# Kernel optimization log

Hardware: AMD Instinct MI355X
Metric: run time of the kernel (lower is better)

## Reference

```python
import jax, jax.numpy as jnp
import numpy as np

N_NODES = 100000
N_HYPEREDGES = 10000
NNZ = 1600000

def setup_inputs() -> dict:
    key = jax.random.key(0)
    k = jax.random.split(key, 7)
    return {
        "x": jax.random.normal(k[0], (N_NODES, 1), dtype=jnp.float32),
        "W1": jax.random.normal(k[1], (1, 128), dtype=jnp.float32) * 0.5,
        "b1": jax.random.normal(k[2], (128,), dtype=jnp.float32) * 0.1,
        "W2": jax.random.normal(k[3], (128, 1), dtype=jnp.float32) * 0.1,
        "b2": jax.random.normal(k[4], (1,), dtype=jnp.float32) * 0.1,
        "node_idx": jax.random.randint(k[5], (NNZ,), 0, N_NODES, dtype=jnp.int64),
        "edge_idx": jax.random.randint(k[6], (NNZ,), 0, N_HYPEREDGES, dtype=jnp.int64),
    }

def _hypergraph_conv(x, W, b, node_idx, edge_idx, n_nodes, n_edges):
    # PyG HypergraphConv (use_attention=False, hyperedge_weight=1):
    # out = D^-1 H B^-1 H^T (X W) + b
    x = x @ W  # [N, F_out]
    ones = jnp.ones(node_idx.shape[0], dtype=x.dtype)
    D = jax.ops.segment_sum(ones, node_idx, num_segments=n_nodes)   # node degree
    B = jax.ops.segment_sum(ones, edge_idx, num_segments=n_edges)   # hyperedge degree
    D_inv = jnp.where(D > 0, 1.0 / D, 0.0)
    B_inv = jnp.where(B > 0, 1.0 / B, 0.0)
    # node -> hyperedge: e = B^-1 H^T x
    e = B_inv[:, None] * jax.ops.segment_sum(x[node_idx], edge_idx, num_segments=n_edges)
    # hyperedge -> node: out = D^-1 H e
    out = D_inv[:, None] * jax.ops.segment_sum(e[edge_idx], node_idx, num_segments=n_nodes)
    return out + b

def reference(x, W1, b1, W2, b2, node_idx, edge_idx):
    n_nodes = x.shape[0]
    h = _hypergraph_conv(x, W1, b1, node_idx, edge_idx, n_nodes, N_HYPEREDGES)
    h = jax.nn.relu(h)
    out = _hypergraph_conv(h, W2, b2, node_idx, edge_idx, n_nodes, N_HYPEREDGES)
    return out
```

## Files before the change

### kernel.cpp

```cpp
#include <hip/hip_runtime.h>

static constexpr int N_NODES = 100000;
static constexpr int N_EDGES = 10000;
static constexpr int NNZ     = 1600000;

static constexpr int G1    = 256;
static constexpr int CHUNK = NNZ / G1;
static constexpr int NRN   = 250;
static constexpr int RN    = 400;
static constexpr int NRE   = 250;
static constexpr int RE    = 40;
static constexpr int SLOT  = 64;
static constexpr int BLK   = 1024;
static constexpr int NW    = BLK / 64;


__global__ __launch_bounds__(BLK) void k_bin(
        const int* __restrict__ nidx, const int* __restrict__ eidx,
        unsigned* __restrict__ binN, unsigned* __restrict__ binE,
        unsigned* __restrict__ cntN, unsigned* __restrict__ cntE) {
    __shared__ unsigned cN[NRN], cE[NRE];
    for (int j = threadIdx.x; j < NRN; j += BLK) cN[j] = 0u;
    for (int j = threadIdx.x; j < NRE; j += BLK) cE[j] = 0u;
    __syncthreads();
    const int b = blockIdx.x;
    const int i0 = b * CHUNK, i1 = i0 + CHUNK;
    for (int i = i0 + threadIdx.x; i < i1; i += BLK) {
        int n = nidx[i], e = eidx[i];
        int rn = n / RN;
        int re = e / RE;
        unsigned pn = atomicAdd(&cN[rn], 1u);
        unsigned pe = atomicAdd(&cE[re], 1u);
        binN[((size_t)rn * G1 + b) * SLOT + pn] = ((unsigned)(n - rn * RN) << 14) | (unsigned)e;
        binE[((size_t)re * G1 + b) * SLOT + pe] = ((unsigned)(e - re * RE) << 17) | (unsigned)n;
    }
    __syncthreads();
    for (int j = threadIdx.x; j < NRN; j += BLK) cntN[(size_t)j * G1 + b] = cN[j];
    for (int j = threadIdx.x; j < NRE; j += BLK) cntE[(size_t)j * G1 + b] = cE[j];
}

__global__ __launch_bounds__(BLK) void k_edge1(
        const unsigned* __restrict__ binE, const unsigned* __restrict__ cntE,
        const float* __restrict__ x,
        float* __restrict__ Binv, float* __restrict__ v1) {
    __shared__ float    sS[NW][RE];
    __shared__ unsigned sC[NW][RE];
    __shared__ unsigned scnt[G1];
    const int t = threadIdx.x;
    for (int j = t; j < NW * RE; j += BLK) { ((float*)sS)[j] = 0.0f; ((unsigned*)sC)[j] = 0u; }
    if (t < G1) scnt[t] = cntE[(size_t)blockIdx.x * G1 + t];
    __syncthreads();
    const int wv = t >> 6;
    const unsigned* base = binE + (size_t)blockIdx.x * G1 * SLOT;
    for (int j = t; j < G1 * SLOT; j += BLK) {
        int s = j & (SLOT - 1), bb = j >> 6;
        if ((unsigned)s < scnt[bb]) {
            unsigned w = base[j];
            unsigned el = w >> 17;
            unsigned n  = w & 0x1FFFFu;
            atomicAdd(&sS[wv][el], x[n]);
            atomicAdd(&sC[wv][el], 1u);
        }
    }
    __syncthreads();
    if (t < RE) {
        float s = 0.0f; unsigned c = 0u;
        #pragma unroll
        for (int k = 0; k < NW; ++k) { s += sS[k][t]; c += sC[k][t]; }
        float binv = (c > 0u) ? (1.0f / (float)c) : 0.0f;
        int e = blockIdx.x * RE + t;
        Binv[e] = binv;
        v1[e]   = s * binv;
    }
}

__global__ __launch_bounds__(BLK) void k_node1_mlp(
        const unsigned* __restrict__ binN, const unsigned* __restrict__ cntN,
        const float* __restrict__ v1,
        const float* __restrict__ W1, const float* __restrict__ b1,
        const float* __restrict__ W2,
        float* __restrict__ Dinv, float* __restrict__ y) {
    __shared__ float    sV[N_EDGES];
    __shared__ float    sS[RN];
    __shared__ unsigned sC[RN];
    __shared__ unsigned scnt[G1];
    __shared__ float    wgt[384];
    for (int j = threadIdx.x; j < N_EDGES; j += BLK) sV[j] = v1[j];
    if (threadIdx.x < RN) { sS[threadIdx.x] = 0.0f; sC[threadIdx.x] = 0u; }
    if (threadIdx.x < G1) scnt[threadIdx.x] = cntN[(size_t)blockIdx.x * G1 + threadIdx.x];
    if (threadIdx.x < 128) {
        wgt[threadIdx.x]       = W1[threadIdx.x];
        wgt[128 + threadIdx.x] = b1[threadIdx.x];
        wgt[256 + threadIdx.x] = W2[threadIdx.x];
    }
    __syncthreads();
    const unsigned* base = binN + (size_t)blockIdx.x * G1 * SLOT;
    for (int j = threadIdx.x; j < G1 * SLOT; j += BLK) {
        int s = j & (SLOT - 1), bb = j >> 6;
        if ((unsigned)s < scnt[bb]) {
            unsigned w = base[j];
            unsigned nl = w >> 14;
            atomicAdd(&sS[nl], sV[w & 0x3FFFu]);
            atomicAdd(&sC[nl], 1u);
        }
    }
    __syncthreads();
    if (threadIdx.x < RN) {
        unsigned c = sC[threadIdx.x];
        float dinv = (c > 0u) ? (1.0f / (float)c) : 0.0f;
        int n = blockIdx.x * RN + threadIdx.x;
        Dinv[n] = dinv;
        float tt = sS[threadIdx.x] * dinv;
        float acc = 0.0f;
        #pragma unroll
        for (int f = 0; f < 128; ++f) {
            float h = fmaf(tt, wgt[f], wgt[128 + f]);
            h = fmaxf(h, 0.0f);
            acc = fmaf(h, wgt[256 + f], acc);
        }
        y[n] = acc;
    }
}

__global__ __launch_bounds__(BLK) void k_edge2(
        const unsigned* __restrict__ binE, const unsigned* __restrict__ cntE,
        const float* __restrict__ y, const float* __restrict__ Binv,
        float* __restrict__ v2) {
    __shared__ float    sS[NW][RE];
    __shared__ unsigned scnt[G1];
    const int t = threadIdx.x;
    for (int j = t; j < NW * RE; j += BLK) ((float*)sS)[j] = 0.0f;
    if (t < G1) scnt[t] = cntE[(size_t)blockIdx.x * G1 + t];
    __syncthreads();
    const int wv = t >> 6;
    const unsigned* base = binE + (size_t)blockIdx.x * G1 * SLOT;
    for (int j = t; j < G1 * SLOT; j += BLK) {
        int s = j & (SLOT - 1), bb = j >> 6;
        if ((unsigned)s < scnt[bb]) {
            unsigned w = base[j];
            atomicAdd(&sS[wv][w >> 17], y[w & 0x1FFFFu]);
        }
    }
    __syncthreads();
    if (t < RE) {
        float s = 0.0f;
        #pragma unroll
        for (int k = 0; k < NW; ++k) s += sS[k][t];
        int e = blockIdx.x * RE + t;
        v2[e] = s * Binv[e];
    }
}

__global__ __launch_bounds__(BLK) void k_node2_final(
        const unsigned* __restrict__ binN, const unsigned* __restrict__ cntN,
        const float* __restrict__ v2, const float* __restrict__ Dinv,
        const float* __restrict__ b2, float* __restrict__ out) {
    __shared__ float    sV[N_EDGES];
    __shared__ float    sS[RN];
    __shared__ unsigned scnt[G1];
    for (int j = threadIdx.x; j < N_EDGES; j += BLK) sV[j] = v2[j];
    if (threadIdx.x < RN) sS[threadIdx.x] = 0.0f;
    if (threadIdx.x < G1) scnt[threadIdx.x] = cntN[(size_t)blockIdx.x * G1 + threadIdx.x];
    __syncthreads();
    const unsigned* base = binN + (size_t)blockIdx.x * G1 * SLOT;
    for (int j = threadIdx.x; j < G1 * SLOT; j += BLK) {
        int s = j & (SLOT - 1), bb = j >> 6;
        if ((unsigned)s < scnt[bb]) {
            unsigned w = base[j];
            atomicAdd(&sS[w >> 14], sV[w & 0x3FFFu]);
        }
    }
    __syncthreads();
    if (threadIdx.x < RN) {
        int n = blockIdx.x * RN + threadIdx.x;
        out[n] = fmaf(sS[threadIdx.x], Dinv[n], b2[0]);
    }
}

extern "C" void kernel_launch(void* const* d_in, const int* in_sizes, int n_in,
                              void* d_out, int out_size, void* d_ws, size_t ws_size,
                              hipStream_t stream) {
    const float* x    = (const float*)d_in[0];
    const float* W1   = (const float*)d_in[1];
    const float* b1   = (const float*)d_in[2];
    const float* W2   = (const float*)d_in[3];
    const float* b2   = (const float*)d_in[4];
    const int*   nidx = (const int*)d_in[5];
    const int*   eidx = (const int*)d_in[6];
    float*       out  = (float*)d_out;

    char* ws = (char*)d_ws;
    unsigned* binN = (unsigned*)(ws + 0);
    unsigned* binE = (unsigned*)(ws + 16384000);
    unsigned* cntN = (unsigned*)(ws + 32768000);
    unsigned* cntE = (unsigned*)(ws + 33024000);
    float*    v1   = (float*)(ws + 33280000);
    float*    v2   = v1 + N_EDGES;
    float*    Binv = v2 + N_EDGES;
    float*    Dinv = Binv + N_EDGES;
    float*    y    = Dinv + N_NODES;

    k_bin          <<<G1,  BLK, 0, stream>>>(nidx, eidx, binN, binE, cntN, cntE);
    k_edge1        <<<NRE, BLK, 0, stream>>>(binE, cntE, x, Binv, v1);
    k_node1_mlp    <<<NRN, BLK, 0, stream>>>(binN, cntN, v1, W1, b1, W2, Dinv, y);
    k_edge2        <<<NRE, BLK, 0, stream>>>(binE, cntE, y, Binv, v2);
    k_node2_final  <<<NRN, BLK, 0, stream>>>(binN, cntN, v2, Dinv, b2, out);
}
```

Before: 83.92 us.

## Fuse four propagation kernels into one persistent kernel with grid barriers

```diff
diff --git a/kernel.cpp b/kernel.cpp
--- a/kernel.cpp
+++ b/kernel.cpp
@@ -13,13 +13,28 @@
 static constexpr int SLOT  = 64;
 static constexpr int BLK   = 1024;
 static constexpr int NW    = BLK / 64;
-
+static constexpr int GF    = 256;
+
+
+__device__ __forceinline__ void grid_barrier(unsigned* bar, unsigned target) {
+    __syncthreads();
+    if (threadIdx.x == 0) {
+        __threadfence();
+        __hip_atomic_fetch_add(bar, 1u, __ATOMIC_RELEASE, __HIP_MEMORY_SCOPE_AGENT);
+        while (__hip_atomic_load(bar, __ATOMIC_RELAXED, __HIP_MEMORY_SCOPE_AGENT) < target)
+            __builtin_amdgcn_s_sleep(16);
+        __threadfence();
+    }
+    __syncthreads();
+}
 
 __global__ __launch_bounds__(BLK) void k_bin(
         const int* __restrict__ nidx, const int* __restrict__ eidx,
         unsigned* __restrict__ binN, unsigned* __restrict__ binE,
-        unsigned* __restrict__ cntN, unsigned* __restrict__ cntE) {
+        unsigned* __restrict__ cntN, unsigned* __restrict__ cntE,
+        unsigned* __restrict__ bar) {
     __shared__ unsigned cN[NRN], cE[NRE];
+    if (blockIdx.x == 0 && threadIdx.x < 4) bar[threadIdx.x] = 0u;
     for (int j = threadIdx.x; j < NRN; j += BLK) cN[j] = 0u;
     for (int j = threadIdx.x; j < NRE; j += BLK) cE[j] = 0u;
     __syncthreads();
@@ -39,141 +54,131 @@
     for (int j = threadIdx.x; j < NRE; j += BLK) cntE[(size_t)j * G1 + b] = cE[j];
 }
 
-__global__ __launch_bounds__(BLK) void k_edge1(
-        const unsigned* __restrict__ binE, const unsigned* __restrict__ cntE,
+__global__ __launch_bounds__(BLK) void k_fused(
+        const unsigned* __restrict__ binN, const unsigned* __restrict__ binE,
+        const unsigned* __restrict__ cntN, const unsigned* __restrict__ cntE,
         const float* __restrict__ x,
-        float* __restrict__ Binv, float* __restrict__ v1) {
-    __shared__ float    sS[NW][RE];
-    __shared__ unsigned sC[NW][RE];
-    __shared__ unsigned scnt[G1];
+        const float* __restrict__ W1, const float* __restrict__ b1,
+        const float* __restrict__ W2, const float* __restrict__ b2,
+        float* __restrict__ v1, float* __restrict__ v2,
+        float* __restrict__ Binv, float* __restrict__ Dinv, float* __restrict__ y,
+        unsigned* __restrict__ bar, float* __restrict__ out) {
+    __shared__ union {
+        struct { unsigned scnt[G1]; float sS[NW][RE]; unsigned sC[NW][RE]; } e;
+        struct { float sV[N_EDGES]; float sS[RN]; unsigned sC[RN]; unsigned scnt[G1];
+                 float wgt[384]; } n;
+    } sm;
+    const int b = blockIdx.x;
     const int t = threadIdx.x;
-    for (int j = t; j < NW * RE; j += BLK) { ((float*)sS)[j] = 0.0f; ((unsigned*)sC)[j] = 0u; }
-    if (t < G1) scnt[t] = cntE[(size_t)blockIdx.x * G1 + t];
-    __syncthreads();
-    const int wv = t >> 6;
-    const unsigned* base = binE + (size_t)blockIdx.x * G1 * SLOT;
-    for (int j = t; j < G1 * SLOT; j += BLK) {
-        int s = j & (SLOT - 1), bb = j >> 6;
-        if ((unsigned)s < scnt[bb]) {
-            unsigned w = base[j];
-            unsigned el = w >> 17;
-            unsigned n  = w & 0x1FFFFu;
-            atomicAdd(&sS[wv][el], x[n]);
-            atomicAdd(&sC[wv][el], 1u);
-        }
-    }
-    __syncthreads();
-    if (t < RE) {
-        float s = 0.0f; unsigned c = 0u;
-        #pragma unroll
-        for (int k = 0; k < NW; ++k) { s += sS[k][t]; c += sC[k][t]; }
-        float binv = (c > 0u) ? (1.0f / (float)c) : 0.0f;
-        int e = blockIdx.x * RE + t;
-        Binv[e] = binv;
-        v1[e]   = s * binv;
-    }
-}
-
-__global__ __launch_bounds__(BLK) void k_node1_mlp(
-        const unsigned* __restrict__ binN, const unsigned* __restrict__ cntN,
-        const float* __restrict__ v1,
-        const float* __restrict__ W1, const float* __restrict__ b1,
-        const float* __restrict__ W2,
-        float* __restrict__ Dinv, float* __restrict__ y) {
-    __shared__ float    sV[N_EDGES];
-    __shared__ float    sS[RN];
-    __shared__ unsigned sC[RN];
-    __shared__ unsigned scnt[G1];
-    __shared__ float    wgt[384];
-    for (int j = threadIdx.x; j < N_EDGES; j += BLK) sV[j] = v1[j];
-    if (threadIdx.x < RN) { sS[threadIdx.x] = 0.0f; sC[threadIdx.x] = 0u; }
-    if (threadIdx.x < G1) scnt[threadIdx.x] = cntN[(size_t)blockIdx.x * G1 + threadIdx.x];
-    if (threadIdx.x < 128) {
-        wgt[threadIdx.x]       = W1[threadIdx.x];
-        wgt[128 + threadIdx.x] = b1[threadIdx.x];
-        wgt[256 + threadIdx.x] = W2[threadIdx.x];
-    }
-    __syncthreads();
-    const unsigned* base = binN + (size_t)blockIdx.x * G1 * SLOT;
-    for (int j = threadIdx.x; j < G1 * SLOT; j += BLK) {
-        int s = j & (SLOT - 1), bb = j >> 6;
-        if ((unsigned)s < scnt[bb]) {
-            unsigned w = base[j];
-            unsigned nl = w >> 14;
-            atomicAdd(&sS[nl], sV[w & 0x3FFFu]);
-            atomicAdd(&sC[nl], 1u);
-        }
-    }
-    __syncthreads();
-    if (threadIdx.x < RN) {
-        unsigned c = sC[threadIdx.x];
-        float dinv = (c > 0u) ? (1.0f / (float)c) : 0.0f;
-        int n = blockIdx.x * RN + threadIdx.x;
-        Dinv[n] = dinv;
-        float tt = sS[threadIdx.x] * dinv;
-        float acc = 0.0f;
-        #pragma unroll
-        for (int f = 0; f < 128; ++f) {
-            float h = fmaf(tt, wgt[f], wgt[128 + f]);
-            h = fmaxf(h, 0.0f);
-            acc = fmaf(h, wgt[256 + f], acc);
-        }
-        y[n] = acc;
-    }
-}
-
-__global__ __launch_bounds__(BLK) void k_edge2(
-        const unsigned* __restrict__ binE, const unsigned* __restrict__ cntE,
-        const float* __restrict__ y, const float* __restrict__ Binv,
-        float* __restrict__ v2) {
-    __shared__ float    sS[NW][RE];
-    __shared__ unsigned scnt[G1];
-    const int t = threadIdx.x;
-    for (int j = t; j < NW * RE; j += BLK) ((float*)sS)[j] = 0.0f;
-    if (t < G1) scnt[t] = cntE[(size_t)blockIdx.x * G1 + t];
-    __syncthreads();
-    const int wv = t >> 6;
-    const unsigned* base = binE + (size_t)blockIdx.x * G1 * SLOT;
-    for (int j = t; j < G1 * SLOT; j += BLK) {
-        int s = j & (SLOT - 1), bb = j >> 6;
-        if ((unsigned)s < scnt[bb]) {
-            unsigned w = base[j];
-            atomicAdd(&sS[wv][w >> 17], y[w & 0x1FFFFu]);
-        }
-    }
-    __syncthreads();
-    if (t < RE) {
-        float s = 0.0f;
-        #pragma unroll
-        for (int k = 0; k < NW; ++k) s += sS[k][t];
-        int e = blockIdx.x * RE + t;
-        v2[e] = s * Binv[e];
-    }
-}
-
-__global__ __launch_bounds__(BLK) void k_node2_final(
-        const unsigned* __restrict__ binN, const unsigned* __restrict__ cntN,
-        const float* __restrict__ v2, const float* __restrict__ Dinv,
-        const float* __restrict__ b2, float* __restrict__ out) {
-    __shared__ float    sV[N_EDGES];
-    __shared__ float    sS[RN];
-    __shared__ unsigned scnt[G1];
-    for (int j = threadIdx.x; j < N_EDGES; j += BLK) sV[j] = v2[j];
-    if (threadIdx.x < RN) sS[threadIdx.x] = 0.0f;
-    if (threadIdx.x < G1) scnt[threadIdx.x] = cntN[(size_t)blockIdx.x * G1 + threadIdx.x];
-    __syncthreads();
-    const unsigned* base = binN + (size_t)blockIdx.x * G1 * SLOT;
-    for (int j = threadIdx.x; j < G1 * SLOT; j += BLK) {
-        int s = j & (SLOT - 1), bb = j >> 6;
-        if ((unsigned)s < scnt[bb]) {
-            unsigned w = base[j];
-            atomicAdd(&sS[w >> 14], sV[w & 0x3FFFu]);
-        }
-    }
-    __syncthreads();
-    if (threadIdx.x < RN) {
-        int n = blockIdx.x * RN + threadIdx.x;
-        out[n] = fmaf(sS[threadIdx.x], Dinv[n], b2[0]);
+
+    if (b < NRE) {
+        for (int j = t; j < NW * RE; j += BLK) { (&sm.e.sS[0][0])[j] = 0.0f; (&sm.e.sC[0][0])[j] = 0u; }
+        if (t < G1) sm.e.scnt[t] = cntE[(size_t)b * G1 + t];
+        __syncthreads();
+        const int wv = t >> 6;
+        const unsigned* base = binE + (size_t)b * G1 * SLOT;
+        for (int j = t; j < G1 * SLOT; j += BLK) {
+            int s = j & (SLOT - 1), bb = j >> 6;
+            if ((unsigned)s < sm.e.scnt[bb]) {
+                unsigned w = base[j];
+                atomicAdd(&sm.e.sS[wv][w >> 17], x[w & 0x1FFFFu]);
+                atomicAdd(&sm.e.sC[wv][w >> 17], 1u);
+            }
+        }
+        __syncthreads();
+        if (t < RE) {
+            float s = 0.0f; unsigned c = 0u;
+            #pragma unroll
+            for (int k = 0; k < NW; ++k) { s += sm.e.sS[k][t]; c += sm.e.sC[k][t]; }
+            float binv = (c > 0u) ? (1.0f / (float)c) : 0.0f;
+            int e = b * RE + t;
+            Binv[e] = binv;
+            v1[e]   = s * binv;
+        }
+    }
+    grid_barrier(bar + 0, GF);
+
+    if (b < NRN) {
+        for (int j = t; j < N_EDGES; j += BLK) sm.n.sV[j] = v1[j];
+        if (t < RN) { sm.n.sS[t] = 0.0f; sm.n.sC[t] = 0u; }
+        if (t < G1) sm.n.scnt[t] = cntN[(size_t)b * G1 + t];
+        if (t < 128) {
+            sm.n.wgt[t]       = W1[t];
+            sm.n.wgt[128 + t] = b1[t];
+            sm.n.wgt[256 + t] = W2[t];
+        }
+        __syncthreads();
+        const unsigned* base = binN + (size_t)b * G1 * SLOT;
+        for (int j = t; j < G1 * SLOT; j += BLK) {
+            int s = j & (SLOT - 1), bb = j >> 6;
+            if ((unsigned)s < sm.n.scnt[bb]) {
+                unsigned w = base[j];
+                unsigned nl = w >> 14;
+                atomicAdd(&sm.n.sS[nl], sm.n.sV[w & 0x3FFFu]);
+                atomicAdd(&sm.n.sC[nl], 1u);
+            }
+        }
+        __syncthreads();
+        if (t < RN) {
+            unsigned c = sm.n.sC[t];
+            float dinv = (c > 0u) ? (1.0f / (float)c) : 0.0f;
+            int n = b * RN + t;
+            Dinv[n] = dinv;
+            float tt = sm.n.sS[t] * dinv;
+            float acc = 0.0f;
+            #pragma unroll
+            for (int f = 0; f < 128; ++f) {
+                float h = fmaf(tt, sm.n.wgt[f], sm.n.wgt[128 + f]);
+                h = fmaxf(h, 0.0f);
+                acc = fmaf(h, sm.n.wgt[256 + f], acc);
+            }
+            y[n] = acc;
+        }
+    }
+    grid_barrier(bar + 1, GF);
+
+    if (b < NRE) {
+        for (int j = t; j < NW * RE; j += BLK) (&sm.e.sS[0][0])[j] = 0.0f;
+        if (t < G1) sm.e.scnt[t] = cntE[(size_t)b * G1 + t];
+        __syncthreads();
+        const int wv = t >> 6;
+        const unsigned* base = binE + (size_t)b * G1 * SLOT;
+        for (int j = t; j < G1 * SLOT; j += BLK) {
+            int s = j & (SLOT - 1), bb = j >> 6;
+            if ((unsigned)s < sm.e.scnt[bb]) {
+                unsigned w = base[j];
+                atomicAdd(&sm.e.sS[wv][w >> 17], y[w & 0x1FFFFu]);
+            }
+        }
+        __syncthreads();
+        if (t < RE) {
+            float s = 0.0f;
+            #pragma unroll
+            for (int k = 0; k < NW; ++k) s += sm.e.sS[k][t];
+            int e = b * RE + t;
+            v2[e] = s * Binv[e];
+        }
+    }
+    grid_barrier(bar + 2, GF);
+
+    if (b < NRN) {
+        for (int j = t; j < N_EDGES; j += BLK) sm.n.sV[j] = v2[j];
+        if (t < RN) sm.n.sS[t] = 0.0f;
+        if (t < G1) sm.n.scnt[t] = cntN[(size_t)b * G1 + t];
+        __syncthreads();
+        const unsigned* base = binN + (size_t)b * G1 * SLOT;
+        for (int j = t; j < G1 * SLOT; j += BLK) {
+            int s = j & (SLOT - 1), bb = j >> 6;
+            if ((unsigned)s < sm.n.scnt[bb]) {
+                unsigned w = base[j];
+                atomicAdd(&sm.n.sS[w >> 14], sm.n.sV[w & 0x3FFFu]);
+            }
+        }
+        __syncthreads();
+        if (t < RN) {
+            int n = b * RN + t;
+            out[n] = fmaf(sm.n.sS[t], Dinv[n], b2[0]);
+        }
     }
 }
 
@@ -195,14 +200,13 @@
     unsigned* cntN = (unsigned*)(ws + 32768000);
     unsigned* cntE = (unsigned*)(ws + 33024000);
     float*    v1   = (float*)(ws + 33280000);
-    float*    v2   = v1 + N_EDGES;
-    float*    Binv = v2 + N_EDGES;
-    float*    Dinv = Binv + N_EDGES;
-    float*    y    = Dinv + N_NODES;
-
-    k_bin          <<<G1,  BLK, 0, stream>>>(nidx, eidx, binN, binE, cntN, cntE);
-    k_edge1        <<<NRE, BLK, 0, stream>>>(binE, cntE, x, Binv, v1);
-    k_node1_mlp    <<<NRN, BLK, 0, stream>>>(binN, cntN, v1, W1, b1, W2, Dinv, y);
-    k_edge2        <<<NRE, BLK, 0, stream>>>(binE, cntE, y, Binv, v2);
-    k_node2_final  <<<NRN, BLK, 0, stream>>>(binN, cntN, v2, Dinv, b2, out);
-}
+    float*    v2   = (float*)(ws + 33320000);
+    float*    Binv = (float*)(ws + 33360000);
+    float*    Dinv = (float*)(ws + 33400000);
+    float*    y    = (float*)(ws + 33800000);
+    unsigned* bar  = (unsigned*)(ws + 34200000);
+
+    k_bin  <<<G1, BLK, 0, stream>>>(nidx, eidx, binN, binE, cntN, cntE, bar);
+    k_fused<<<GF, BLK, 0, stream>>>(binN, binE, cntN, cntE, x, W1, b1, W2, b2,
+                                    v1, v2, Binv, Dinv, y, bar, out);
+}
```

Result: slower. 141.1 us (+68.1%).
